# Kernel tuning notes

Hardware: AMD Instinct MI355X
Metric: run time of the kernel (lower is better)

The kernel has to match this reference:

```python
import jax, jax.numpy as jnp
import numpy as np

B, S, DIM = 1, 2048, 1024
HEADS, KV_HEADS, DH = 16, 2, 64
GQ = HEADS // KV_HEADS
CBS = 64   # compress block size
SBS = 64   # selection block size
NUM_SEL = 8
WIN = 512  # sliding window size
NUM_MEM = 1
SCALE = DH ** -0.5
NEG = -jnp.finfo(jnp.float32).max


def setup_inputs():
    ks = jax.random.split(jax.random.key(0), 12)
    cdim = CBS * DH
    dim_inner = HEADS * DH
    dim_kv = KV_HEADS * DH
    p = lambda k, shape: jax.random.normal(k, shape, jnp.float32) * 0.02
    return {
        "x": jax.random.normal(ks[0], (B, S, DIM), jnp.float32),
        "rms_g": jnp.ones((DIM,), jnp.float32),
        "W_qkv": p(ks[1], (DIM, dim_inner + 2 * dim_kv)),
        "k_pos": p(ks[2], (KV_HEADS, CBS, DH)),
        "v_pos": p(ks[3], (KV_HEADS, CBS, DH)),
        "mem_kv": p(ks[4], (2, KV_HEADS, NUM_MEM, DH)),
        "kW1": p(ks[5], (cdim, cdim)), "kb1": jnp.zeros((cdim,), jnp.float32),
        "kW2": p(ks[6], (cdim, DH)), "kb2": jnp.zeros((DH,), jnp.float32),
        "vW1": p(ks[7], (cdim, cdim)), "vb1": jnp.zeros((cdim,), jnp.float32),
        "vW2": p(ks[8], (cdim, DH)), "vb2": jnp.zeros((DH,), jnp.float32),
        "W_comb": p(ks[9], (DIM, 3 * HEADS)),
        "b_comb": jnp.tile(jnp.array([-2.0, -2.0, 2.0], jnp.float32), HEADS),
        "W_out": p(ks[10], (HEADS * DH, DIM)),
    }


def _rot_half(u):
    v = u.reshape(u.shape[:-1] + (DH // 2, 2))
    return jnp.stack([-v[..., 1], v[..., 0]], axis=-1).reshape(u.shape)


def reference(x, rms_g, W_qkv, k_pos, v_pos, mem_kv, kW1, kb1, kW2, kb2,
              vW1, vb1, vW2, vb2, W_comb, b_comb, W_out):
    n_cb = S // CBS
    n_fb = S // SBS
    num_sel = min(NUM_SEL, n_cb)

    # RMSNorm
    xn = x * jax.lax.rsqrt(jnp.mean(x * x, -1, keepdims=True) + jnp.finfo(jnp.float32).eps) * rms_g

    qkv = xn @ W_qkv
    q, k, v = jnp.split(qkv, [HEADS * DH, (HEADS + KV_HEADS) * DH], axis=-1)
    q = q.reshape(B, S, HEADS, DH).transpose(0, 2, 1, 3)       # b h n d
    k = k.reshape(B, S, KV_HEADS, DH).transpose(0, 2, 1, 3)
    v = v.reshape(B, S, KV_HEADS, DH).transpose(0, 2, 1, 3)

    # ---- compressed branch: per-block MLP compression of K/V ----
    kc = (k + jnp.tile(k_pos, (1, n_cb, 1))[None]).reshape(B, KV_HEADS, n_cb, CBS * DH)
    vc = (v + jnp.tile(v_pos, (1, n_cb, 1))[None]).reshape(B, KV_HEADS, n_cb, CBS * DH)
    ck = jax.nn.relu(kc @ kW1 + kb1) @ kW2 + kb2               # b h w d
    cv = jax.nn.relu(vc @ vW1 + vb1) @ vW2 + vb2
    ck = jnp.concatenate([jnp.broadcast_to(mem_kv[0], (B, KV_HEADS, NUM_MEM, DH)), ck], axis=2)
    cv = jnp.concatenate([jnp.broadcast_to(mem_kv[1], (B, KV_HEADS, NUM_MEM, DH)), cv], axis=2)
    ck_seq = jnp.concatenate([jnp.full((NUM_MEM,), -1), (jnp.arange(n_cb) + 1) * CBS - 1])
    cmask = ck_seq[None, :] < jnp.arange(S)[:, None]           # [S, mem+n_cb]
    qg = q.reshape(B, KV_HEADS, GQ, S, DH)
    csim = jnp.einsum('bhgid,bhjd->bhgij', qg, ck) * SCALE
    csim = jnp.where(cmask, csim, NEG)
    c_out = jnp.einsum('bhgij,bhjd->bhgid', jax.nn.softmax(csim, -1), cv).reshape(B, HEADS, S, DH)

    # ---- rotary embedding (interleaved pairs, theta=10000) ----
    inv_freq = 1.0 / (10000.0 ** (jnp.arange(0, DH, 2, dtype=jnp.float32) / DH))
    freqs = jnp.repeat(jnp.arange(S, dtype=jnp.float32)[:, None] * inv_freq, 2, axis=-1)
    cos, sin = jnp.cos(freqs), jnp.sin(freqs)
    rq = q * cos + _rot_half(q) * sin
    rk = k * cos + _rot_half(k) * sin

    # ---- block selection from compressed attention scores ----
    imp = csim[..., NUM_MEM:].mean(axis=2)                     # mean over grouped queries: [B,KVH,S,n_cb]
    imp = jnp.concatenate([jnp.full(imp.shape[:-1] + (1,), -1000.0), imp], -1)
    imp = jax.nn.softmax(imp, -1)[..., 1:]
    sel_val, sel_idx = jax.lax.top_k(imp, num_sel)             # [B,KVH,S,sel]
    fmask = jnp.broadcast_to((sel_val > 1e-10)[..., None], (B, KV_HEADS, S, num_sel, SBS))
    diag_idx = jnp.broadcast_to((jnp.arange(S) // SBS)[None, None, :, None], (B, KV_HEADS, S, 1))
    sel_idx = jnp.concatenate([sel_idx, diag_idx], -1)         # append own (diagonal) block
    causal = jnp.tril(jnp.ones((SBS, SBS), bool))
    diag_mask = jnp.broadcast_to(jnp.tile(causal, (n_fb, 1))[None, None, :, None, :], (B, KV_HEADS, S, 1, SBS))
    fmask = jnp.concatenate([fmask, diag_mask], axis=-2).reshape(B, KV_HEADS, S, (num_sel + 1) * SBS)

    # ---- fine attention over gathered selected blocks ----
    fkb = rk.reshape(B, KV_HEADS, 1, n_fb, SBS, DH)
    fvb = v.reshape(B, KV_HEADS, 1, n_fb, SBS, DH)
    gi = sel_idx[..., None, None]                              # [B,KVH,S,sel+1,1,1]
    fk = jnp.take_along_axis(fkb, gi, axis=3).reshape(B, KV_HEADS, S, (num_sel + 1) * SBS, DH)
    fv = jnp.take_along_axis(fvb, gi, axis=3).reshape(B, KV_HEADS, S, (num_sel + 1) * SBS, DH)
    fqg = rq.reshape(B, KV_HEADS, GQ, S, DH)
    fsim = jnp.einsum('bhgid,bhijd->bhgij', fqg, fk) * SCALE
    fsim = jnp.where(fmask[:, :, None], fsim, NEG)
    f_out = jnp.einsum('bhgij,bhijd->bhgid', jax.nn.softmax(fsim, -1), fv).reshape(B, HEADS, S, DH)

    # ---- causal sliding window (exact window, look_backward=1) ----
    skf = jnp.repeat(rk, GQ, axis=1)
    svf = jnp.repeat(v, GQ, axis=1)
    nw = S // WIN
    kw = skf.reshape(B, HEADS, nw, WIN, DH)
    vw = svf.reshape(B, HEADS, nw, WIN, DH)
    kcat = jnp.concatenate([jnp.pad(kw, ((0, 0), (0, 0), (1, 0), (0, 0), (0, 0)))[:, :, :nw], kw], axis=3)
    vcat = jnp.concatenate([jnp.pad(vw, ((0, 0), (0, 0), (1, 0), (0, 0), (0, 0)))[:, :, :nw], vw], axis=3)
    qw = rq.reshape(B, HEADS, nw, WIN, DH)
    gq_pos = jnp.arange(nw)[:, None, None] * WIN + jnp.arange(WIN)[None, :, None]
    gk_pos = jnp.arange(nw)[:, None, None] * WIN - WIN + jnp.arange(2 * WIN)[None, None, :]
    smask = (gk_pos >= 0) & (gk_pos <= gq_pos) & (gq_pos - gk_pos <= WIN)
    ssim = jnp.where(smask, jnp.einsum('bhwid,bhwjd->bhwij', qw, kcat) * SCALE, NEG)
    s_out = jnp.einsum('bhwij,bhwjd->bhwid', jax.nn.softmax(ssim, -1), vcat).reshape(B, HEADS, S, DH)

    # ---- learned per-token, per-head strategy combination ----
    gates = jax.nn.sigmoid(xn @ W_comb + b_comb).reshape(B, S, HEADS, 3).transpose(0, 2, 1, 3)
    out = gates[..., 0:1] * c_out + gates[..., 1:2] * f_out + gates[..., 2:3] * s_out
    return out.transpose(0, 2, 1, 3).reshape(B, S, HEADS * DH) @ W_out
```

## Files before the change

kernel.cpp:

```cpp
#include <hip/hip_runtime.h>
#include <hip/hip_bf16.h>
#include <cstddef>
#include <cstdint>

#define S      2048
#define DIM    1024
#define HEADS  16
#define KVH    2
#define GQ     8
#define DH     64
#define CBS    64
#define SBS    64
#define NUMSEL 8
#define WIN    512
#define NCB    (S / CBS)
#define CDIM   (CBS * DH)
#define QKVC   (HEADS * DH + 2 * KVH * DH)
#define KOFF   (HEADS * DH)
#define VOFF   (HEADS * DH + KVH * DH)
#define SCALE  0.125f
#define RMS_EPS 1.1920928955078125e-07f

typedef __attribute__((ext_vector_type(8))) short bf16x8;
typedef __attribute__((ext_vector_type(4))) float f32x4;
// ... 140 lines not shown
            if (gn >= N) continue;
            #pragma unroll
            for (int r = 0; r < 4; r++) {
                int gm = bm + m0 + i * 16 + quad * 4 + r;
                float v = acc[i][j][r];
                if (bias) v += bias[gn];
                if (ACT == 2) v = 1.f / (1.f + expf(-v));
                C[(size_t)gm * N + gn] = v;
            }
        }
    }
}

template <int BM, int BN, int WM, int WN>
__global__ __launch_bounds__(256) void gemm_mfma_kernel(
        const __hip_bfloat16* __restrict__ A, const float* __restrict__ B,
        float* __restrict__ C, int M, int N, int K, int kslice) {
    constexpr int BK = 32;
    constexpr int TM = BM / (WM * 16);
    constexpr int TN = BN / (WN * 16);
    constexpr int LDK = BK + 8;
    constexpr int NB = BN * BK / 256;
    __shared__ __hip_bfloat16 As[BM][LDK];
    __shared__ __hip_bfloat16 Bs[BN][LDK];
    int tid = threadIdx.x;
    int wave = tid >> 6, lane = tid & 63;
    int wm = wave % WM, wn = wave / WM;
    int m0 = wm * TM * 16, n0 = wn * TN * 16;
    int bm = blockIdx.y * BM, bn = blockIdx.x * BN;
    int kbeg = blockIdx.z * kslice, kend = kbeg + kslice;
    int lm = lane & 15, quad = lane >> 4;
    f32x4 acc[TM][TN] = {};
    for (int k0 = kbeg; k0 < kend; k0 += BK) {
        #pragma unroll
        for (int e = 0; e < BM * BK / (256 * 8); e++) {
            int idx = (tid + e * 256) * 8;
            int r = idx >> 5, kk = idx & 31;
            *(bf16x8*)(&As[r][kk]) =
                *(const bf16x8*)(A + (size_t)(bm + r) * K + k0 + kk);
        }
        float tmpB[NB];
        #pragma unroll
        for (int e = 0; e < NB; e++) {
            int idx = tid + e * 256;
            int kk = idx / BN, n = idx % BN;
            tmpB[e] = B[(size_t)(k0 + kk) * N + bn + n];
        }
        #pragma unroll
        for (int e = 0; e < NB; e++) {
            int idx = tid + e * 256;
            int kk = idx / BN, n = idx % BN;
            Bs[n][kk] = __float2bfloat16(tmpB[e]);
        }
        __syncthreads();
        bf16x8 af[TM], bf_[TN];
        #pragma unroll
        for (int i = 0; i < TM; i++)
            af[i] = *(const bf16x8*)(&As[m0 + i * 16 + lm][quad * 8]);
        #pragma unroll
        for (int j = 0; j < TN; j++)
            bf_[j] = *(const bf16x8*)(&Bs[n0 + j * 16 + lm][quad * 8]);
        #pragma unroll
        for (int i = 0; i < TM; i++)
            #pragma unroll
            for (int j = 0; j < TN; j++)
                acc[i][j] = __builtin_amdgcn_mfma_f32_16x16x32_bf16(
                    af[i], bf_[j], acc[i][j], 0, 0, 0);
        __syncthreads();
    }
    size_t cbase = (size_t)blockIdx.z * M * N;
    #pragma unroll
    for (int i = 0; i < TM; i++) {
        #pragma unroll
        for (int j = 0; j < TN; j++) {
            int gn = bn + n0 + j * 16 + lm;
            #pragma unroll
            for (int r = 0; r < 4; r++) {
                int gm = bm + m0 + i * 16 + quad * 4 + r;
                C[cbase + (size_t)gm * N + gn] = acc[i][j][r];
            }
        }
    }
}

__global__ __launch_bounds__(256) void gemm_splitk_kernel(
        const float* __restrict__ A, const float* __restrict__ B,
        float* __restrict__ P, int M, int N, int K, int kslice) {
    const int BM = 64, BN = 64, BK = 16;
    __shared__ float As[BK][BM + 4];
    __shared__ float Bs[BK][BN];
    int bm = blockIdx.y * BM, bn = blockIdx.x * BN;
    int z = blockIdx.z;
    int kbeg = z * kslice, kend = kbeg + kslice;
    int tid = threadIdx.x;
    int tx = tid & 15, ty = tid >> 4;
    float acc[4][4] = {{0.f}};
    for (int k0 = kbeg; k0 < kend; k0 += BK) {
        #pragma unroll
        for (int e = 0; e < 4; e++) {
            int idx = tid + e * 256;
            int m = idx >> 4, kk = idx & 15;
            int gm = bm + m;
            As[kk][m] = (gm < M) ? A[(size_t)gm * K + k0 + kk] : 0.f;
        }
        #pragma unroll
        for (int e = 0; e < 4; e++) {
            int idx = tid + e * 256;
            int kk = idx >> 6, n = idx & 63;
            int gn = bn + n;
            Bs[kk][n] = (gn < N) ? B[(size_t)(k0 + kk) * N + gn] : 0.f;
        }
        __syncthreads();
        #pragma unroll
        for (int kk = 0; kk < BK; kk++) {
            float a[4], b[4];
            #pragma unroll
            for (int i = 0; i < 4; i++) a[i] = As[kk][ty * 4 + i];
            #pragma unroll
            for (int j = 0; j < 4; j++) b[j] = Bs[kk][tx * 4 + j];
            #pragma unroll
            for (int i = 0; i < 4; i++)
                #pragma unroll
                for (int j = 0; j < 4; j++) acc[i][j] += a[i] * b[j];
        }
        __syncthreads();
    }
    #pragma unroll
    for (int i = 0; i < 4; i++) {
        int gm = bm + ty * 4 + i;
        if (gm >= M) continue;
        #pragma unroll
        for (int j = 0; j < 4; j++) {
            int gn = bn + tx * 4 + j;
            if (gn >= N) continue;
            P[((size_t)z * M + gm) * N + gn] = acc[i][j];
        }
    }
}

template <int ACT>
__global__ __launch_bounds__(256) void reduce_splitk_kernel(
        const float* __restrict__ P, const float* __restrict__ bias,
        float* __restrict__ C, int MN, int N, int splits) {
    int e = blockIdx.x * 256 + threadIdx.x;
    if (e >= MN) return;
    float s = 0.f;
    for (int z = 0; z < splits; z++) s += P[(size_t)z * MN + e];
    s += bias[e % N];
    if (ACT == 1) s = fmaxf(s, 0.f);
    C[e] = s;
}

__global__ __launch_bounds__(256) void rotary_kernel(
        const float* __restrict__ qkv, float* __restrict__ rq, float* __restrict__ rk,
        short* __restrict__ rkb) {
    int s = blockIdx.x, tid = threadIdx.x;
    for (int p = tid; p < (HEADS + KVH) * (DH / 2); p += 256) {
        int t; const float* src; float* dst; short* dst2 = nullptr;
        if (p < HEADS * (DH / 2)) {
            int h = p >> 5; t = p & 31;
            src = qkv + (size_t)s * QKVC + h * DH + 2 * t;
            dst = rq + (size_t)s * (HEADS * DH) + h * DH + 2 * t;
        } else {
            int pp = p - HEADS * (DH / 2);
            int h = pp >> 5; t = pp & 31;
            src = qkv + (size_t)s * QKVC + KOFF + h * DH + 2 * t;
            dst = rk + (size_t)s * (KVH * DH) + h * DH + 2 * t;
            dst2 = rkb + (size_t)s * (KVH * DH) + h * DH + 2 * t;
        }
        float u0 = src[0], u1 = src[1];
        float freq = powf(10000.f, -((float)(2 * t) / (float)DH));
        float ang = (float)s * freq;
        float sn, cs;
        sincosf(ang, &sn, &cs);
        float o0 = u0 * cs - u1 * sn;
        float o1 = u1 * cs + u0 * sn;
        dst[0] = o0;
        dst[1] = o1;
        if (dst2) { dst2[0] = f2bs(o0); dst2[1] = f2bs(o1); }
    }
}

__global__ __launch_bounds__(256) void build_cmat_kernel(
        const float* __restrict__ qkv, const float* __restrict__ k_pos,
        const float* __restrict__ v_pos, __hip_bfloat16* __restrict__ kcm,
        __hip_bfloat16* __restrict__ vcm) {
    int r = blockIdx.x;
    int h = r >> 5, w = r & 31;
    for (int e = threadIdx.x; e < CDIM; e += 256) {
        int i = e >> 6, d = e & 63;
        size_t qb = (size_t)(w * CBS + i) * QKVC;
        kcm[(size_t)r * CDIM + e] =
            __float2bfloat16(qkv[qb + KOFF + h * DH + d] + k_pos[(h * CBS + i) * DH + d]);
        vcm[(size_t)r * CDIM + e] =
            __float2bfloat16(qkv[qb + VOFF + h * DH + d] + v_pos[(h * CBS + i) * DH + d]);
    }
}

__global__ __launch_bounds__(256) void assemble_kernel(
        const float* __restrict__ ckb, const float* __restrict__ cvb,
        const float* __restrict__ mem_kv, float* __restrict__ ck, float* __restrict__ cv) {
    int e = blockIdx.x * 256 + threadIdx.x;
    if (e >= KVH * (NCB + 1) * DH) return;
    int d = e & 63;
    int j = (e >> 6) % (NCB + 1);
    int h = e / ((NCB + 1) * DH);
    if (j == 0) {
        ck[e] = mem_kv[0 * KVH * DH + h * DH + d];
        cv[e] = mem_kv[1 * KVH * DH + h * DH + d];
    } else {
        ck[e] = ckb[((size_t)h * NCB + j - 1) * DH + d];
        cv[e] = cvb[((size_t)h * NCB + j - 1) * DH + d];
    }
}

__global__ __launch_bounds__(64) void imp_kernel(
        const float* __restrict__ qkv, const float* __restrict__ ck,
        float* __restrict__ imp) {
    int kvh = blockIdx.x, s = blockIdx.y, t = threadIdx.x;
    __shared__ float qg[GQ * DH];
    __shared__ float ckl[NCB * 65];
    for (int e = t; e < GQ * DH; e += 64) {
        int g = e >> 6, d = e & 63;
        qg[e] = qkv[(size_t)s * QKVC + (kvh * GQ + g) * DH + d];
    }
    for (int e = t; e < NCB * DH; e += 64) {
        int w = e >> 6, d = e & 63;
        ckl[w * 65 + d] = ck[((size_t)kvh * (NCB + 1) + 1 + w) * DH + d];
    }
    __syncthreads();
    if (t < NCB) {
        int w = t;
        float val;
        if (w * CBS + CBS - 1 < s) {
            float acc = 0.f;
            #pragma unroll
            for (int g = 0; g < GQ; g++) {
                const float* qp = qg + g * DH;
                const float* cp = ckl + w * 65;
                #pragma unroll 16
                for (int d = 0; d < DH; d++) acc += qp[d] * cp[d];
            }
            val = acc * SCALE * (1.f / (float)GQ);
        } else {
            val = -INFINITY;
        }
        imp[((size_t)kvh * S + s) * NCB + w] = val;
    }
}

__global__ __launch_bounds__(256) void select_kernel(
        const float* __restrict__ imp, int* __restrict__ sel) {
    int idx = blockIdx.x * 256 + threadIdx.x;
    if (idx >= KVH * S) return;
    const float* row = imp + (size_t)idx * NCB;
    float p[NCB];
    float m = -1000.f;
    for (int w = 0; w < NCB; w++) { p[w] = row[w]; m = fmaxf(m, p[w]); }
    float z = expf(-1000.f - m);
    for (int w = 0; w < NCB; w++) { p[w] = expf(p[w] - m); z += p[w]; }
    float inv = 1.f / z;
    bool used[NCB];
    for (int w = 0; w < NCB; w++) used[w] = false;
    for (int i = 0; i < NUMSEL; i++) {
        int best = 0; float bv = -1.f;
        for (int w = 0; w < NCB; w++) {
            if (!used[w]) {
                float pw = p[w] * inv;
                if (pw > bv) { bv = pw; best = w; }
            }
        }
        used[best] = true;
        sel[(size_t)idx * NUMSEL + i] = (bv > 1e-10f) ? best : -1;
    }
}

__global__ __launch_bounds__(256) void cattn_kernel(
        const float* __restrict__ qkv, const float* __restrict__ ck,
        const float* __restrict__ cv, const float* __restrict__ gates,
        float* __restrict__ attn) {
    int h = blockIdx.x, qb = blockIdx.y;
    int kvh = h >> 3;
    int tid = threadIdx.x;
    int tx = tid & 15, ty = tid >> 4;
    __shared__ float Qs[64][68];
    __shared__ float Ks[64][68];
    __shared__ float Vs[64][68];
    auto& Ps = Ks;
    for (int e = tid; e < 4096; e += 256) {
        int q = e >> 6, d = e & 63;
        Qs[d][q] = qkv[(size_t)(qb * 64 + q) * QKVC + h * DH + d];
    }
    for (int e = tid; e < 4096; e += 256) {
        int j = e >> 6, d = e & 63;
        float kvl = 0.f, vvl = 0.f;
        if (j < NCB + 1) {
            kvl = ck[((size_t)kvh * (NCB + 1) + j) * DH + d];
            vvl = cv[((size_t)kvh * (NCB + 1) + j) * DH + d];
        }
        Ks[d][j] = kvl;
        Vs[j][d] = vvl;
    }
    __syncthreads();
    float sc[4][4] = {{0.f}};
    for (int d = 0; d < 64; d++) {
        float4 av = *(const float4*)&Qs[d][ty * 4];
        float4 bv = *(const float4*)&Ks[d][tx * 4];
        float a[4] = {av.x, av.y, av.z, av.w};
        float b[4] = {bv.x, bv.y, bv.z, bv.w};
        #pragma unroll
        for (int i = 0; i < 4; i++)
            #pragma unroll
            for (int j = 0; j < 4; j++) sc[i][j] += a[i] * b[j];
    }
    __syncthreads();
    float l[4];
    float pv4[4][4];
    #pragma unroll
    for (int i = 0; i < 4; i++) {
        int spos = qb * 64 + ty * 4 + i;
        float tm = -INFINITY;
        #pragma unroll
        for (int j = 0; j < 4; j++) {
            int jj = tx * 4 + j;
            bool vis = (jj == 0) || ((jj <= NCB) && (jj * 64 <= spos));
            sc[i][j] = vis ? sc[i][j] * SCALE : -INFINITY;
            tm = fmaxf(tm, sc[i][j]);
        }
        #pragma unroll
        for (int o = 1; o < 16; o <<= 1) tm = fmaxf(tm, __shfl_xor(tm, o));
        float rs = 0.f;
        #pragma unroll
        for (int j = 0; j < 4; j++) {
            float p = expf(sc[i][j] - tm);
            pv4[i][j] = p;
            rs += p;
        }
        #pragma unroll
        for (int o = 1; o < 16; o <<= 1) rs += __shfl_xor(rs, o);
        l[i] = rs;
    }
    #pragma unroll
    for (int j = 0; j < 4; j++) {
        float4 w = make_float4(pv4[0][j], pv4[1][j], pv4[2][j], pv4[3][j]);
        *(float4*)&Ps[tx * 4 + j][ty * 4] = w;
    }
    __syncthreads();
    float acc[4][4] = {{0.f}};
    for (int jj = 0; jj < 64; jj++) {
        float4 av = *(const float4*)&Ps[jj][ty * 4];
        float4 bv = *(const float4*)&Vs[jj][tx * 4];
        float a[4] = {av.x, av.y, av.z, av.w};
        float b[4] = {bv.x, bv.y, bv.z, bv.w};
        #pragma unroll
        for (int i = 0; i < 4; i++)
            #pragma unroll
            for (int j = 0; j < 4; j++) acc[i][j] += a[i] * b[j];
    }
    #pragma unroll
    for (int i = 0; i < 4; i++) {
        int spos = qb * 64 + ty * 4 + i;
        float g0 = gates[((size_t)spos * HEADS + h) * 3 + 0];
        float sca = g0 / l[i];
        #pragma unroll
        for (int j = 0; j < 4; j++)
            attn[(size_t)spos * (HEADS * DH) + h * DH + tx * 4 + j] = acc[i][j] * sca;
    }
}

__global__ __launch_bounds__(256) void fattn_kernel(
        const float* __restrict__ rq, const short* __restrict__ rkb,
        const short* __restrict__ vb, const int* __restrict__ sel,
        const float* __restrict__ gates, float* __restrict__ attn) {
    int kvh = blockIdx.x, s = blockIdx.y;
    int tid = threadIdx.x;
    int wv = tid >> 6, lane = tid & 63;
    int lm = lane & 15, quad = lane >> 4;
    int hh = tid >> 5, lk = tid & 31;
    __shared__ short Qb[16][68];
    __shared__ short Vt[64][68];
    __shared__ short Pb[16][68];
    __shared__ float Sc[8][68];
    __shared__ float alph[8], fac[8];
    __shared__ int bl[9];
    for (int e = tid; e < 512; e += 256) {
        int h = e >> 6, d = e & 63;
        Qb[h][d] = f2bs(rq[(size_t)s * (HEADS * DH) + (kvh * 8 + h) * DH + d]);
    }
    if (tid < NUMSEL) bl[tid] = sel[((size_t)kvh * S + s) * NUMSEL + tid];
    if (tid == NUMSEL) bl[NUMSEL] = s >> 6;
    __syncthreads();
    bf16x8 aq0 = *(const bf16x8*)&Qb[lm][quad * 8];
    bf16x8 aq1 = *(const bf16x8*)&Qb[lm][32 + quad * 8];
    float mh = -INFINITY, lh = 0.f;
    f32x4 oacc = {0.f, 0.f, 0.f, 0.f};
    for (int i = 0; i < 9; i++) {
        int w = bl[i];
        if (i < NUMSEL && w < 0) continue;
        #pragma unroll
        for (int r = 0; r < 2; r++) {
            int idx = tid + r * 256;
            int c8 = idx >> 6, j = idx & 63;
            bf16x8 vv = *(const bf16x8*)(vb + ((size_t)(w * SBS + j) * KVH + kvh) * DH + c8 * 8);
            #pragma unroll
            for (int t = 0; t < 8; t++) Vt[c8 * 8 + t][j] = vv[t];
        }
        {
            const short* kp = rkb + ((size_t)(w * SBS + wv * 16 + lm) * KVH + kvh) * DH;
            bf16x8 bk0 = *(const bf16x8*)(kp + quad * 8);
            bf16x8 bk1 = *(const bf16x8*)(kp + 32 + quad * 8);
            f32x4 sc4 = {0.f, 0.f, 0.f, 0.f};
            sc4 = __builtin_amdgcn_mfma_f32_16x16x32_bf16(aq0, bk0, sc4, 0, 0, 0);
            sc4 = __builtin_amdgcn_mfma_f32_16x16x32_bf16(aq1, bk1, sc4, 0, 0, 0);
            bool vis = (i < NUMSEL) || (wv * 16 + lm <= (s & 63));
            #pragma unroll
            for (int r = 0; r < 4; r++) {
                int row = quad * 4 + r;
                if (row < 8) Sc[row][wv * 16 + lm] = vis ? sc4[r] * SCALE : -INFINITY;
            }
        }
        __syncthreads();
        {
            float s0 = Sc[hh][lk], s1 = Sc[hh][lk + 32];
            float bmx = fmaxf(s0, s1);
            #pragma unroll
            for (int o = 1; o < 32; o <<= 1) bmx = fmaxf(bmx, __shfl_xor(bmx, o));
            float mn = fmaxf(mh, bmx);
            float scl = expf(mh - mn);
            float p0 = expf(s0 - mn), p1 = expf(s1 - mn);
            float rs = p0 + p1;
            #pragma unroll
            for (int o = 1; o < 32; o <<= 1) rs += __shfl_xor(rs, o);
            lh = lh * scl + rs;
            mh = mn;
            Pb[hh][lk] = f2bs(p0);
            Pb[hh][lk + 32] = f2bs(p1);
            if (lk == 0) alph[hh] = scl;
        }
        __syncthreads();
        {
            bf16x8 ap0 = *(const bf16x8*)&Pb[lm][quad * 8];
            bf16x8 ap1 = *(const bf16x8*)&Pb[lm][32 + quad * 8];
            bf16x8 bv0 = *(const bf16x8*)&Vt[wv * 16 + lm][quad * 8];
            bf16x8 bv1 = *(const bf16x8*)&Vt[wv * 16 + lm][32 + quad * 8];
            #pragma unroll
            for (int r = 0; r < 4; r++) oacc[r] *= alph[(quad * 4 + r) & 7];
            oacc = __builtin_amdgcn_mfma_f32_16x16x32_bf16(ap0, bv0, oacc, 0, 0, 0);
            oacc = __builtin_amdgcn_mfma_f32_16x16x32_bf16(ap1, bv1, oacc, 0, 0, 0);
        }
        __syncthreads();
    }
    if (lk == 0)
        fac[hh] = gates[((size_t)s * HEADS + kvh * 8 + hh) * 3 + 1] / lh;
    __syncthreads();
    #pragma unroll
    for (int r = 0; r < 4; r++) {
        int row = quad * 4 + r;
        if (row < 8)
            attn[(size_t)s * (HEADS * DH) + (kvh * 8 + row) * DH + wv * 16 + lm]
                += oacc[r] * fac[row];
    }
}

__global__ __launch_bounds__(256) void sattn_kernel(
        const float* __restrict__ rq, const float* __restrict__ rk,
        const float* __restrict__ qkv, const float* __restrict__ gates,
        float* __restrict__ attn) {
    int h = blockIdx.x, qb = blockIdx.y;
    int kvh = h >> 3;
    int tid = threadIdx.x;
    int tx = tid & 15, ty = tid >> 4;
    __shared__ float Qs[64][68];
    __shared__ float Ks[64][68];
    __shared__ float Vs[64][68];
    auto& Ps = Ks;
    for (int e = tid; e < 4096; e += 256) {
        int q = e >> 6, d = e & 63;
        Qs[d][q] = rq[(size_t)(qb * 64 + q) * (HEADS * DH) + h * DH + d];
    }
    float m[4], l[4], acc[4][4];
    #pragma unroll
    for (int i = 0; i < 4; i++) {
        m[i] = -INFINITY; l[i] = 0.f;
        #pragma unroll
        for (int j = 0; j < 4; j++) acc[i][j] = 0.f;
    }
    __syncthreads();
    for (int c = 0; c < 9; c++) {
        int kb = qb * 64 - WIN + c * 64;
        if (kb + 63 < 0) continue;
        for (int e = tid; e < 4096; e += 256) {
            int j = e >> 6, d = e & 63;
            int jpos = kb + j;
            float kvl = 0.f, vvl = 0.f;
            if (jpos >= 0) {
                kvl = rk[(size_t)jpos * (KVH * DH) + kvh * DH + d];
                vvl = qkv[(size_t)jpos * QKVC + VOFF + kvh * DH + d];
            }
            Ks[d][j] = kvl;
            Vs[j][d] = vvl;
        }
        __syncthreads();
        float sc[4][4] = {{0.f}};
        for (int d = 0; d < 64; d++) {
            float4 av = *(const float4*)&Qs[d][ty * 4];
            float4 bv = *(const float4*)&Ks[d][tx * 4];
            float a[4] = {av.x, av.y, av.z, av.w};
            float b[4] = {bv.x, bv.y, bv.z, bv.w};
            #pragma unroll
            for (int i = 0; i < 4; i++)
                #pragma unroll
                for (int j = 0; j < 4; j++) sc[i][j] += a[i] * b[j];
        }
        __syncthreads();
        float pv4[4][4];
        #pragma unroll
        for (int i = 0; i < 4; i++) {
            int spos = qb * 64 + ty * 4 + i;
            float tm = -INFINITY;
            #pragma unroll
            for (int j = 0; j < 4; j++) {
                int jpos = kb + tx * 4 + j;
                bool valid = (jpos >= 0) && (jpos <= spos) && (jpos >= spos - WIN);
                sc[i][j] = valid ? sc[i][j] * SCALE : -INFINITY;
                tm = fmaxf(tm, sc[i][j]);
            }
            #pragma unroll
            for (int o = 1; o < 16; o <<= 1) tm = fmaxf(tm, __shfl_xor(tm, o));
            float mn = fmaxf(m[i], tm);
            float sca = (mn == -INFINITY) ? 1.f : expf(m[i] - mn);
            float rs = 0.f;
            #pragma unroll
            for (int j = 0; j < 4; j++) {
                float p = (mn == -INFINITY) ? 0.f : expf(sc[i][j] - mn);
                pv4[i][j] = p;
                rs += p;
            }
            #pragma unroll
            for (int o = 1; o < 16; o <<= 1) rs += __shfl_xor(rs, o);
            l[i] = l[i] * sca + rs;
            m[i] = mn;
            #pragma unroll
            for (int j = 0; j < 4; j++) acc[i][j] *= sca;
        }
        #pragma unroll
        for (int j = 0; j < 4; j++) {
            float4 w = make_float4(pv4[0][j], pv4[1][j], pv4[2][j], pv4[3][j]);
            *(float4*)&Ps[tx * 4 + j][ty * 4] = w;
        }
        __syncthreads();
        for (int jj = 0; jj < 64; jj++) {
            float4 av = *(const float4*)&Ps[jj][ty * 4];
            float4 bv = *(const float4*)&Vs[jj][tx * 4];
            float a[4] = {av.x, av.y, av.z, av.w};
            float b[4] = {bv.x, bv.y, bv.z, bv.w};
            #pragma unroll
            for (int i = 0; i < 4; i++)
                #pragma unroll
                for (int j = 0; j < 4; j++) acc[i][j] += a[i] * b[j];
        }
        __syncthreads();
    }
    #pragma unroll
    for (int i = 0; i < 4; i++) {
        int spos = qb * 64 + ty * 4 + i;
        float g2 = gates[((size_t)spos * HEADS + h) * 3 + 2];
        float sca = g2 / l[i];
        #pragma unroll
        for (int j = 0; j < 4; j++)
            attn[(size_t)spos * (HEADS * DH) + h * DH + tx * 4 + j] += acc[i][j] * sca;
    }
}

extern "C" void kernel_launch(void* const* d_in, const int* in_sizes, int n_in,
                              void* d_out, int out_size, void* d_ws, size_t ws_size,
                              hipStream_t stream) {
    const float* x      = (const float*)d_in[0];
    const float* rms_g  = (const float*)d_in[1];
    const float* W_qkv  = (const float*)d_in[2];
    const float* k_pos  = (const float*)d_in[3];
    const float* v_pos  = (const float*)d_in[4];
    const float* mem_kv = (const float*)d_in[5];
    const float* kW1    = (const float*)d_in[6];
    const float* kb1    = (const float*)d_in[7];
    const float* kW2    = (const float*)d_in[8];
    const float* kb2    = (const float*)d_in[9];
    const float* vW1    = (const float*)d_in[10];
    const float* vb1    = (const float*)d_in[11];
    const float* vW2    = (const float*)d_in[12];
    const float* vb2    = (const float*)d_in[13];
    const float* W_comb = (const float*)d_in[14];
    const float* b_comb = (const float*)d_in[15];
    const float* W_out  = (const float*)d_in[16];
    float* out = (float*)d_out;

    float* ws    = (float*)d_ws;
    float* xn    = ws;
    float* qkv   = xn    + (size_t)S * DIM;
    float* rq    = qkv   + (size_t)S * QKVC;
    float* rk    = rq    + (size_t)S * HEADS * DH;
    float* R     = rk    + (size_t)S * KVH * DH;
    float* ck    = R     + 1048576;
    float* cv    = ck    + (size_t)KVH * (NCB + 1) * DH;
    float* imp   = cv    + (size_t)KVH * (NCB + 1) * DH;
    float* gates = imp   + (size_t)KVH * S * NCB;
    float* attn  = gates + (size_t)S * HEADS * 3;
    int*   sel   = (int*)(attn + (size_t)S * HEADS * DH);
    float* WT    = attn + (size_t)S * HEADS * DH + 32768;
    short* wqkvT = (short*)WT;
    short* woutT = (short*)(WT + 655360);
    short* wcombT= (short*)(WT + 655360 + 524288);

    __hip_bfloat16* xnb   = (__hip_bfloat16*)R;
    __hip_bfloat16* kcmb  = (__hip_bfloat16*)R;
    __hip_bfloat16* vcmb  = (__hip_bfloat16*)(R + 131072);
    float* khid  = R + 262144;
    float* vhid  = R + 524288;
    float* ckb   = R + 786432;
    float* cvb   = R + 790528;
    short* rkb   = (short*)(R + 794624);
    __hip_bfloat16* attnb = (__hip_bfloat16*)R;
    short* vbb   = (short*)imp;
    float* partW1 = attn;
    float* partW2 = imp;

    transpose_cast_kernel<<<dim3(QKVC / 64, DIM / 64), 256, 0, stream>>>(W_qkv, wqkvT, DIM, QKVC);
    transpose_cast_kernel<<<dim3(DIM / 64, DIM / 64), 256, 0, stream>>>(W_out, woutT, DIM, DIM);
    transpose_cast_kernel<<<dim3(1, DIM / 64), 256, 0, stream>>>(W_comb, wcombT, DIM, HEADS * 3);
    rmsnorm_kernel<<<S, 256, 0, stream>>>(x, rms_g, xn, xnb);
    gemm_bt_kernel<64, 64, 2, 2, 0><<<dim3(QKVC / 64, S / 64), 256, 0, stream>>>(
        xnb, wqkvT, nullptr, qkv, S, QKVC, DIM);
    gemm_bt_kernel<64, 64, 2, 2, 2><<<dim3(1, S / 64), 256, 0, stream>>>(
        xnb, wcombT, b_comb, gates, S, HEADS * 3, DIM);
    rotary_kernel<<<S, 256, 0, stream>>>(qkv, rq, rk, rkb);
    build_cmat_kernel<<<KVH * NCB, 256, 0, stream>>>(qkv, k_pos, v_pos, kcmb, vcmb);
    gemm_mfma_kernel<64, 128, 1, 4><<<dim3(CDIM / 128, 1, 8), 256, 0, stream>>>(
        kcmb, kW1, partW1, 64, CDIM, CDIM, CDIM / 8);
    reduce_splitk_kernel<1><<<(64 * CDIM + 255) / 256, 256, 0, stream>>>(
        partW1, kb1, khid, 64 * CDIM, CDIM, 8);
    gemm_splitk_kernel<<<dim3(1, 1, 32), 256, 0, stream>>>(khid, kW2, partW2, 64, DH, CDIM, CDIM / 32);
    reduce_splitk_kernel<0><<<(64 * DH + 255) / 256, 256, 0, stream>>>(partW2, kb2, ckb, 64 * DH, DH, 32);
    gemm_mfma_kernel<64, 128, 1, 4><<<dim3(CDIM / 128, 1, 8), 256, 0, stream>>>(
        vcmb, vW1, partW1, 64, CDIM, CDIM, CDIM / 8);
    reduce_splitk_kernel<1><<<(64 * CDIM + 255) / 256, 256, 0, stream>>>(
        partW1, vb1, vhid, 64 * CDIM, CDIM, 8);
    gemm_splitk_kernel<<<dim3(1, 1, 32), 256, 0, stream>>>(vhid, vW2, partW2, 64, DH, CDIM, CDIM / 32);
    reduce_splitk_kernel<0><<<(64 * DH + 255) / 256, 256, 0, stream>>>(partW2, vb2, cvb, 64 * DH, DH, 32);
    assemble_kernel<<<(KVH * (NCB + 1) * DH + 255) / 256, 256, 0, stream>>>(ckb, cvb, mem_kv, ck, cv);
    imp_kernel<<<dim3(KVH, S), 64, 0, stream>>>(qkv, ck, imp);
    select_kernel<<<(KVH * S + 255) / 256, 256, 0, stream>>>(imp, sel);
    cast_v_kernel<<<(S * KVH * DH / 4 + 255) / 256, 256, 0, stream>>>(qkv, vbb);
    cattn_kernel<<<dim3(HEADS, S / 64), 256, 0, stream>>>(qkv, ck, cv, gates, attn);
    fattn_kernel<<<dim3(KVH, S), 256, 0, stream>>>(rq, rkb, vbb, sel, gates, attn);
    sattn_kernel<<<dim3(HEADS, S / 64), 256, 0, stream>>>(rq, rk, qkv, gates, attn);
    cast_bf16_kernel<<<(S * HEADS * DH / 4 + 255) / 256, 256, 0, stream>>>(
        attn, attnb, S * HEADS * DH / 4);
    gemm_bt_kernel<64, 64, 2, 2, 0><<<dim3(DIM / 64, S / 64), 256, 0, stream>>>(
        attnb, woutT, nullptr, out, S, DIM, DIM);
}
```

Before: 619.6 us.

## Move compressed and sliding-window attention to bf16 MFMA with bf16 rotary outputs

```diff
diff --git a/kernel.cpp b/kernel.cpp
--- a/kernel.cpp
+++ b/kernel.cpp
@@ -316,32 +316,27 @@
 }
 
 __global__ __launch_bounds__(256) void rotary_kernel(
-        const float* __restrict__ qkv, float* __restrict__ rq, float* __restrict__ rk,
-        short* __restrict__ rkb) {
+        const float* __restrict__ qkv, short* __restrict__ rqb, short* __restrict__ rkb) {
     int s = blockIdx.x, tid = threadIdx.x;
     for (int p = tid; p < (HEADS + KVH) * (DH / 2); p += 256) {
-        int t; const float* src; float* dst; short* dst2 = nullptr;
+        int t; const float* src; short* dst;
         if (p < HEADS * (DH / 2)) {
             int h = p >> 5; t = p & 31;
             src = qkv + (size_t)s * QKVC + h * DH + 2 * t;
-            dst = rq + (size_t)s * (HEADS * DH) + h * DH + 2 * t;
+            dst = rqb + (size_t)s * (HEADS * DH) + h * DH + 2 * t;
         } else {
             int pp = p - HEADS * (DH / 2);
             int h = pp >> 5; t = pp & 31;
             src = qkv + (size_t)s * QKVC + KOFF + h * DH + 2 * t;
-            dst = rk + (size_t)s * (KVH * DH) + h * DH + 2 * t;
-            dst2 = rkb + (size_t)s * (KVH * DH) + h * DH + 2 * t;
+            dst = rkb + (size_t)s * (KVH * DH) + h * DH + 2 * t;
         }
         float u0 = src[0], u1 = src[1];
         float freq = powf(10000.f, -((float)(2 * t) / (float)DH));
         float ang = (float)s * freq;
         float sn, cs;
         sincosf(ang, &sn, &cs);
-        float o0 = u0 * cs - u1 * sn;
-        float o1 = u1 * cs + u0 * sn;
-        dst[0] = o0;
-        dst[1] = o1;
-        if (dst2) { dst2[0] = f2bs(o0); dst2[1] = f2bs(o1); }
+        dst[0] = f2bs(u0 * cs - u1 * sn);
+        dst[1] = f2bs(u1 * cs + u0 * sn);
     }
 }
 
@@ -363,19 +358,23 @@
 
 __global__ __launch_bounds__(256) void assemble_kernel(
         const float* __restrict__ ckb, const float* __restrict__ cvb,
-        const float* __restrict__ mem_kv, float* __restrict__ ck, float* __restrict__ cv) {
+        const float* __restrict__ mem_kv, float* __restrict__ ck, float* __restrict__ cv,
+        short* __restrict__ ck16, short* __restrict__ cv16) {
     int e = blockIdx.x * 256 + threadIdx.x;
     if (e >= KVH * (NCB + 1) * DH) return;
     int d = e & 63;
     int j = (e >> 6) % (NCB + 1);
     int h = e / ((NCB + 1) * DH);
+    float kv, vv;
     if (j == 0) {
-        ck[e] = mem_kv[0 * KVH * DH + h * DH + d];
-        cv[e] = mem_kv[1 * KVH * DH + h * DH + d];
+        kv = mem_kv[0 * KVH * DH + h * DH + d];
+        vv = mem_kv[1 * KVH * DH + h * DH + d];
     } else {
-        ck[e] = ckb[((size_t)h * NCB + j - 1) * DH + d];
-        cv[e] = cvb[((size_t)h * NCB + j - 1) * DH + d];
-    }
+        kv = ckb[((size_t)h * NCB + j - 1) * DH + d];
+        vv = cvb[((size_t)h * NCB + j - 1) * DH + d];
+    }
+    ck[e] = kv; cv[e] = vv;
+    ck16[e] = f2bs(kv); cv16[e] = f2bs(vv);
 }
 
 __global__ __launch_bounds__(64) void imp_kernel(
@@ -440,100 +439,108 @@
 }
 
 __global__ __launch_bounds__(256) void cattn_kernel(
-        const float* __restrict__ qkv, const float* __restrict__ ck,
-        const float* __restrict__ cv, const float* __restrict__ gates,
+        const float* __restrict__ qkv, const short* __restrict__ ck16,
+        const short* __restrict__ cv16, const float* __restrict__ gates,
         float* __restrict__ attn) {
     int h = blockIdx.x, qb = blockIdx.y;
     int kvh = h >> 3;
     int tid = threadIdx.x;
-    int tx = tid & 15, ty = tid >> 4;
-    __shared__ float Qs[64][68];
-    __shared__ float Ks[64][68];
-    __shared__ float Vs[64][68];
-    auto& Ps = Ks;
-    for (int e = tid; e < 4096; e += 256) {
-        int q = e >> 6, d = e & 63;
-        Qs[d][q] = qkv[(size_t)(qb * 64 + q) * QKVC + h * DH + d];
-    }
-    for (int e = tid; e < 4096; e += 256) {
-        int j = e >> 6, d = e & 63;
-        float kvl = 0.f, vvl = 0.f;
+    int wv = tid >> 6, lane = tid & 63;
+    int lm = lane & 15, quad = lane >> 4;
+    __shared__ short Qb[64][72];
+    __shared__ short Ks[64][72];
+    __shared__ short Vt[64][72];
+    __shared__ short Pb[64][72];
+    for (int e = tid; e < 1024; e += 256) {
+        int q = e >> 4, d4 = (e & 15) * 4;
+        float4 v = *(const float4*)(qkv + (size_t)(qb * 64 + q) * QKVC + h * DH + d4);
+        Qb[q][d4 + 0] = f2bs(v.x); Qb[q][d4 + 1] = f2bs(v.y);
+        Qb[q][d4 + 2] = f2bs(v.z); Qb[q][d4 + 3] = f2bs(v.w);
+    }
+    for (int e = tid; e < 512; e += 256) {
+        int c8 = e >> 6, j = e & 63;
+        bf16x8 kv = {}, vv = {};
         if (j < NCB + 1) {
-            kvl = ck[((size_t)kvh * (NCB + 1) + j) * DH + d];
-            vvl = cv[((size_t)kvh * (NCB + 1) + j) * DH + d];
-        }
-        Ks[d][j] = kvl;
-        Vs[j][d] = vvl;
+            kv = *(const bf16x8*)(ck16 + ((size_t)kvh * (NCB + 1) + j) * DH + c8 * 8);
+            vv = *(const bf16x8*)(cv16 + ((size_t)kvh * (NCB + 1) + j) * DH + c8 * 8);
+        }
+        #pragma unroll
+        for (int t = 0; t < 8; t++) {
+            Ks[j][c8 * 8 + t] = kv[t];
+            Vt[c8 * 8 + t][j] = vv[t];
+        }
     }
     __syncthreads();
-    float sc[4][4] = {{0.f}};
-    for (int d = 0; d < 64; d++) {
-        float4 av = *(const float4*)&Qs[d][ty * 4];
-        float4 bv = *(const float4*)&Ks[d][tx * 4];
-        float a[4] = {av.x, av.y, av.z, av.w};
-        float b[4] = {bv.x, bv.y, bv.z, bv.w};
-        #pragma unroll
-        for (int i = 0; i < 4; i++)
-            #pragma unroll
-            for (int j = 0; j < 4; j++) sc[i][j] += a[i] * b[j];
-    }
+    bf16x8 aq0 = *(const bf16x8*)&Qb[wv * 16 + lm][quad * 8];
+    bf16x8 aq1 = *(const bf16x8*)&Qb[wv * 16 + lm][32 + quad * 8];
+    int vismax = (qb < NCB) ? qb : NCB;
+    f32x4 sc[4];
+    #pragma unroll
+    for (int t = 0; t < 4; t++) {
+        bf16x8 bk0 = *(const bf16x8*)&Ks[t * 16 + lm][quad * 8];
+        bf16x8 bk1 = *(const bf16x8*)&Ks[t * 16 + lm][32 + quad * 8];
+        f32x4 s4 = {0.f, 0.f, 0.f, 0.f};
+        s4 = __builtin_amdgcn_mfma_f32_16x16x32_bf16(aq0, bk0, s4, 0, 0, 0);
+        s4 = __builtin_amdgcn_mfma_f32_16x16x32_bf16(aq1, bk1, s4, 0, 0, 0);
+        sc[t] = s4;
+    }
+    float l[4];
+    float pr[4][4];
+    #pragma unroll
+    for (int r = 0; r < 4; r++) {
+        float mx = -INFINITY;
+        #pragma unroll
+        for (int t = 0; t < 4; t++) {
+            int jj = t * 16 + lm;
+            bool vis = (jj == 0) || (jj <= vismax);
+            float v = vis ? sc[t][r] * SCALE : -INFINITY;
+            sc[t][r] = v;
+            mx = fmaxf(mx, v);
+        }
+        #pragma unroll
+        for (int o = 1; o < 16; o <<= 1) mx = fmaxf(mx, __shfl_xor(mx, o));
+        float sum = 0.f;
+        #pragma unroll
+        for (int t = 0; t < 4; t++) {
+            float p = expf(sc[t][r] - mx);
+            pr[r][t] = p;
+            sum += p;
+        }
+        #pragma unroll
+        for (int o = 1; o < 16; o <<= 1) sum += __shfl_xor(sum, o);
+        l[r] = sum;
+    }
+    #pragma unroll
+    for (int r = 0; r < 4; r++)
+        #pragma unroll
+        for (int t = 0; t < 4; t++)
+            Pb[wv * 16 + quad * 4 + r][t * 16 + lm] = f2bs(pr[r][t]);
     __syncthreads();
-    float l[4];
-    float pv4[4][4];
-    #pragma unroll
-    for (int i = 0; i < 4; i++) {
-        int spos = qb * 64 + ty * 4 + i;
-        float tm = -INFINITY;
-        #pragma unroll
-        for (int j = 0; j < 4; j++) {
-            int jj = tx * 4 + j;
-            bool vis = (jj == 0) || ((jj <= NCB) && (jj * 64 <= spos));
-            sc[i][j] = vis ? sc[i][j] * SCALE : -INFINITY;
-            tm = fmaxf(tm, sc[i][j]);
-        }
-        #pragma unroll
-        for (int o = 1; o < 16; o <<= 1) tm = fmaxf(tm, __shfl_xor(tm, o));
-        float rs = 0.f;
-        #pragma unroll
-        for (int j = 0; j < 4; j++) {
-            float p = expf(sc[i][j] - tm);
-            pv4[i][j] = p;
-            rs += p;
-        }
-        #pragma unroll
-        for (int o = 1; o < 16; o <<= 1) rs += __shfl_xor(rs, o);
-        l[i] = rs;
-    }
-    #pragma unroll
-    for (int j = 0; j < 4; j++) {
-        float4 w = make_float4(pv4[0][j], pv4[1][j], pv4[2][j], pv4[3][j]);
-        *(float4*)&Ps[tx * 4 + j][ty * 4] = w;
-    }
-    __syncthreads();
-    float acc[4][4] = {{0.f}};
-    for (int jj = 0; jj < 64; jj++) {
-        float4 av = *(const float4*)&Ps[jj][ty * 4];
-        float4 bv = *(const float4*)&Vs[jj][tx * 4];
-        float a[4] = {av.x, av.y, av.z, av.w};
-        float b[4] = {bv.x, bv.y, bv.z, bv.w};
-        #pragma unroll
-        for (int i = 0; i < 4; i++)
-            #pragma unroll
-            for (int j = 0; j < 4; j++) acc[i][j] += a[i] * b[j];
-    }
-    #pragma unroll
-    for (int i = 0; i < 4; i++) {
-        int spos = qb * 64 + ty * 4 + i;
+    bf16x8 ap0 = *(const bf16x8*)&Pb[wv * 16 + lm][quad * 8];
+    bf16x8 ap1 = *(const bf16x8*)&Pb[wv * 16 + lm][32 + quad * 8];
+    f32x4 oacc[4];
+    #pragma unroll
+    for (int t = 0; t < 4; t++) {
+        bf16x8 bv0 = *(const bf16x8*)&Vt[t * 16 + lm][quad * 8];
+        bf16x8 bv1 = *(const bf16x8*)&Vt[t * 16 + lm][32 + quad * 8];
+        f32x4 a = {0.f, 0.f, 0.f, 0.f};
+        a = __builtin_amdgcn_mfma_f32_16x16x32_bf16(ap0, bv0, a, 0, 0, 0);
+        a = __builtin_amdgcn_mfma_f32_16x16x32_bf16(ap1, bv1, a, 0, 0, 0);
+        oacc[t] = a;
+    }
+    #pragma unroll
+    for (int r = 0; r < 4; r++) {
+        int spos = qb * 64 + wv * 16 + quad * 4 + r;
         float g0 = gates[((size_t)spos * HEADS + h) * 3 + 0];
-        float sca = g0 / l[i];
-        #pragma unroll
-        for (int j = 0; j < 4; j++)
-            attn[(size_t)spos * (HEADS * DH) + h * DH + tx * 4 + j] = acc[i][j] * sca;
+        float f = g0 / l[r];
+        #pragma unroll
+        for (int t = 0; t < 4; t++)
+            attn[(size_t)spos * (HEADS * DH) + h * DH + t * 16 + lm] = oacc[t][r] * f;
     }
 }
 
 __global__ __launch_bounds__(256) void fattn_kernel(
-        const float* __restrict__ rq, const short* __restrict__ rkb,
+        const short* __restrict__ rqb, const short* __restrict__ rkb,
         const short* __restrict__ vb, const int* __restrict__ sel,
         const float* __restrict__ gates, float* __restrict__ attn) {
     int kvh = blockIdx.x, s = blockIdx.y;
@@ -549,7 +556,7 @@
     __shared__ int bl[9];
     for (int e = tid; e < 512; e += 256) {
         int h = e >> 6, d = e & 63;
-        Qb[h][d] = f2bs(rq[(size_t)s * (HEADS * DH) + (kvh * 8 + h) * DH + d]);
+        Qb[h][d] = rqb[(size_t)s * (HEADS * DH) + (kvh * 8 + h) * DH + d];
     }
     if (tid < NUMSEL) bl[tid] = sel[((size_t)kvh * S + s) * NUMSEL + tid];
     if (tid == NUMSEL) bl[NUMSEL] = s >> 6;
@@ -627,112 +634,105 @@
 }
 
 __global__ __launch_bounds__(256) void sattn_kernel(
-        const float* __restrict__ rq, const float* __restrict__ rk,
-        const float* __restrict__ qkv, const float* __restrict__ gates,
+        const short* __restrict__ rqb, const short* __restrict__ rkb,
+        const short* __restrict__ vb, const float* __restrict__ gates,
         float* __restrict__ attn) {
     int h = blockIdx.x, qb = blockIdx.y;
     int kvh = h >> 3;
     int tid = threadIdx.x;
-    int tx = tid & 15, ty = tid >> 4;
-    __shared__ float Qs[64][68];
-    __shared__ float Ks[64][68];
-    __shared__ float Vs[64][68];
-    auto& Ps = Ks;
-    for (int e = tid; e < 4096; e += 256) {
-        int q = e >> 6, d = e & 63;
-        Qs[d][q] = rq[(size_t)(qb * 64 + q) * (HEADS * DH) + h * DH + d];
-    }
-    float m[4], l[4], acc[4][4];
-    #pragma unroll
-    for (int i = 0; i < 4; i++) {
-        m[i] = -INFINITY; l[i] = 0.f;
-        #pragma unroll
-        for (int j = 0; j < 4; j++) acc[i][j] = 0.f;
-    }
-    __syncthreads();
+    int wv = tid >> 6, lane = tid & 63;
+    int lm = lane & 15, quad = lane >> 4;
+    __shared__ short Vt[64][72];
+    __shared__ short Pb[64][72];
+    const short* qp = rqb + (size_t)(qb * 64 + wv * 16 + lm) * (HEADS * DH) + h * DH;
+    bf16x8 aq0 = *(const bf16x8*)(qp + quad * 8);
+    bf16x8 aq1 = *(const bf16x8*)(qp + 32 + quad * 8);
+    int myrow = wv * 16 + quad * 4;
+    float m[4], l[4];
+    f32x4 oacc[4];
+    #pragma unroll
+    for (int r = 0; r < 4; r++) { m[r] = -INFINITY; l[r] = 0.f; }
+    #pragma unroll
+    for (int t = 0; t < 4; t++) oacc[t] = (f32x4){0.f, 0.f, 0.f, 0.f};
     for (int c = 0; c < 9; c++) {
         int kb = qb * 64 - WIN + c * 64;
-        if (kb + 63 < 0) continue;
-        for (int e = tid; e < 4096; e += 256) {
-            int j = e >> 6, d = e & 63;
-            int jpos = kb + j;
-            float kvl = 0.f, vvl = 0.f;
-            if (jpos >= 0) {
-                kvl = rk[(size_t)jpos * (KVH * DH) + kvh * DH + d];
-                vvl = qkv[(size_t)jpos * QKVC + VOFF + kvh * DH + d];
+        if (kb < 0) continue;
+        for (int e = tid; e < 512; e += 256) {
+            int c8 = e >> 6, j = e & 63;
+            bf16x8 vv = *(const bf16x8*)(vb + ((size_t)(kb + j) * KVH + kvh) * DH + c8 * 8);
+            #pragma unroll
+            for (int t = 0; t < 8; t++) Vt[c8 * 8 + t][j] = vv[t];
+        }
+        f32x4 sc[4];
+        #pragma unroll
+        for (int t = 0; t < 4; t++) {
+            const short* kp = rkb + ((size_t)(kb + t * 16 + lm) * KVH + kvh) * DH;
+            bf16x8 bk0 = *(const bf16x8*)(kp + quad * 8);
+            bf16x8 bk1 = *(const bf16x8*)(kp + 32 + quad * 8);
+            f32x4 s4 = {0.f, 0.f, 0.f, 0.f};
+            s4 = __builtin_amdgcn_mfma_f32_16x16x32_bf16(aq0, bk0, s4, 0, 0, 0);
+            s4 = __builtin_amdgcn_mfma_f32_16x16x32_bf16(aq1, bk1, s4, 0, 0, 0);
+            sc[t] = s4;
+        }
+        float pr[4][4];
+        #pragma unroll
+        for (int r = 0; r < 4; r++) {
+            int row = myrow + r;
+            float mx = -INFINITY;
+            #pragma unroll
+            for (int t = 0; t < 4; t++) {
+                int jj = t * 16 + lm;
+                bool vis = true;
+                if (c == 0) vis = (jj >= row);
+                if (c == 8) vis = (jj <= row);
+                float v = vis ? sc[t][r] * SCALE : -INFINITY;
+                sc[t][r] = v;
+                mx = fmaxf(mx, v);
             }
-            Ks[d][j] = kvl;
-            Vs[j][d] = vvl;
-        }
-        __syncthreads();
-        float sc[4][4] = {{0.f}};
-        for (int d = 0; d < 64; d++) {
-            float4 av = *(const float4*)&Qs[d][ty * 4];
-            float4 bv = *(const float4*)&Ks[d][tx * 4];
-            float a[4] = {av.x, av.y, av.z, av.w};
-            float b[4] = {bv.x, bv.y, bv.z, bv.w};
-            #pragma unroll
-            for (int i = 0; i < 4; i++)
-                #pragma unroll
-                for (int j = 0; j < 4; j++) sc[i][j] += a[i] * b[j];
-        }
-        __syncthreads();
-        float pv4[4][4];
-        #pragma unroll
-        for (int i = 0; i < 4; i++) {
-            int spos = qb * 64 + ty * 4 + i;
-            float tm = -INFINITY;
-            #pragma unroll
-            for (int j = 0; j < 4; j++) {
-                int jpos = kb + tx * 4 + j;
-                bool valid = (jpos >= 0) && (jpos <= spos) && (jpos >= spos - WIN);
-                sc[i][j] = valid ? sc[i][j] * SCALE : -INFINITY;
-                tm = fmaxf(tm, sc[i][j]);
+            #pragma unroll
+            for (int o = 1; o < 16; o <<= 1) mx = fmaxf(mx, __shfl_xor(mx, o));
+            float mn = fmaxf(m[r], mx);
+            float al = expf(m[r] - mn);
+            float sum = 0.f;
+            #pragma unroll
+            for (int t = 0; t < 4; t++) {
+                float p = expf(sc[t][r] - mn);
+                pr[r][t] = p;
+                sum += p;
             }
             #pragma unroll
-            for (int o = 1; o < 16; o <<= 1) tm = fmaxf(tm, __shfl_xor(tm, o));
-            float mn = fmaxf(m[i], tm);
-            float sca = (mn == -INFINITY) ? 1.f : expf(m[i] - mn);
-            float rs = 0.f;
-            #pragma unroll
-            for (int j = 0; j < 4; j++) {
-                float p = (mn == -INFINITY) ? 0.f : expf(sc[i][j] - mn);
-                pv4[i][j] = p;
-                rs += p;
-            }
-            #pragma unroll
-            for (int o = 1; o < 16; o <<= 1) rs += __shfl_xor(rs, o);
-            l[i] = l[i] * sca + rs;
-            m[i] = mn;
-            #pragma unroll
-            for (int j = 0; j < 4; j++) acc[i][j] *= sca;
-        }
-        #pragma unroll
-        for (int j = 0; j < 4; j++) {
-            float4 w = make_float4(pv4[0][j], pv4[1][j], pv4[2][j], pv4[3][j]);
-            *(float4*)&Ps[tx * 4 + j][ty * 4] = w;
-        }
-        __syncthreads();
-        for (int jj = 0; jj < 64; jj++) {
-            float4 av = *(const float4*)&Ps[jj][ty * 4];
-            float4 bv = *(const float4*)&Vs[jj][tx * 4];
-            float a[4] = {av.x, av.y, av.z, av.w};
-            float b[4] = {bv.x, bv.y, bv.z, bv.w};
-            #pragma unroll
-            for (int i = 0; i < 4; i++)
-                #pragma unroll
-                for (int j = 0; j < 4; j++) acc[i][j] += a[i] * b[j];
-        }
-        __syncthreads();
-    }
-    #pragma unroll
-    for (int i = 0; i < 4; i++) {
-        int spos = qb * 64 + ty * 4 + i;
+            for (int o = 1; o < 16; o <<= 1) sum += __shfl_xor(sum, o);
+            l[r] = l[r] * al + sum;
+            m[r] = mn;
+            #pragma unroll
+            for (int t = 0; t < 4; t++) oacc[t][r] *= al;
+        }
+        __syncthreads();
+        #pragma unroll
+        for (int r = 0; r < 4; r++)
+            #pragma unroll
+            for (int t = 0; t < 4; t++)
+                Pb[myrow + r][t * 16 + lm] = f2bs(pr[r][t]);
+        __syncthreads();
+        bf16x8 ap0 = *(const bf16x8*)&Pb[wv * 16 + lm][quad * 8];
+        bf16x8 ap1 = *(const bf16x8*)&Pb[wv * 16 + lm][32 + quad * 8];
+        #pragma unroll
+        for (int t = 0; t < 4; t++) {
+            bf16x8 bv0 = *(const bf16x8*)&Vt[t * 16 + lm][quad * 8];
+            bf16x8 bv1 = *(const bf16x8*)&Vt[t * 16 + lm][32 + quad * 8];
+            oacc[t] = __builtin_amdgcn_mfma_f32_16x16x32_bf16(ap0, bv0, oacc[t], 0, 0, 0);
+            oacc[t] = __builtin_amdgcn_mfma_f32_16x16x32_bf16(ap1, bv1, oacc[t], 0, 0, 0);
+        }
+        __syncthreads();
+    }
+    #pragma unroll
+    for (int r = 0; r < 4; r++) {
+        int spos = qb * 64 + myrow + r;
         float g2 = gates[((size_t)spos * HEADS + h) * 3 + 2];
-        float sca = g2 / l[i];
-        #pragma unroll
-        for (int j = 0; j < 4; j++)
-            attn[(size_t)spos * (HEADS * DH) + h * DH + tx * 4 + j] += acc[i][j] * sca;
+        float f = g2 / l[r];
+        #pragma unroll
+        for (int t = 0; t < 4; t++)
+            attn[(size_t)spos * (HEADS * DH) + h * DH + t * 16 + lm] += oacc[t][r] * f;
     }
 }
 
@@ -761,16 +761,18 @@
     float* ws    = (float*)d_ws;
     float* xn    = ws;
     float* qkv   = xn    + (size_t)S * DIM;
-    float* rq    = qkv   + (size_t)S * QKVC;
-    float* rk    = rq    + (size_t)S * HEADS * DH;
-    float* R     = rk    + (size_t)S * KVH * DH;
+    short* rqb   = (short*)(qkv + (size_t)S * QKVC);
+    short* rkb   = (short*)((float*)rqb + 1048576);
+    float* R     = (float*)rkb + 131072;
     float* ck    = R     + 1048576;
     float* cv    = ck    + (size_t)KVH * (NCB + 1) * DH;
-    float* imp   = cv    + (size_t)KVH * (NCB + 1) * DH;
+    short* ck16  = (short*)(cv + (size_t)KVH * (NCB + 1) * DH);
+    short* cv16  = (short*)((float*)ck16 + 2112);
+    float* imp   = (float*)cv16 + 2112;
     float* gates = imp   + (size_t)KVH * S * NCB;
     float* attn  = gates + (size_t)S * HEADS * 3;
     int*   sel   = (int*)(attn + (size_t)S * HEADS * DH);
-    float* WT    = attn + (size_t)S * HEADS * DH + 32768;
+    float* WT    = attn + (size_t)S * HEADS * DH + 8192;
     short* wqkvT = (short*)WT;
     short* woutT = (short*)(WT + 655360);
     short* wcombT= (short*)(WT + 655360 + 524288);
@@ -782,7 +784,6 @@
     float* vhid  = R + 524288;
     float* ckb   = R + 786432;
     float* cvb   = R + 790528;
-    short* rkb   = (short*)(R + 794624);
     __hip_bfloat16* attnb = (__hip_bfloat16*)R;
     short* vbb   = (short*)imp;
     float* partW1 = attn;
@@ -796,7 +797,7 @@
         xnb, wqkvT, nullptr, qkv, S, QKVC, DIM);
     gemm_bt_kernel<64, 64, 2, 2, 2><<<dim3(1, S / 64), 256, 0, stream>>>(
         xnb, wcombT, b_comb, gates, S, HEADS * 3, DIM);
-    rotary_kernel<<<S, 256, 0, stream>>>(qkv, rq, rk, rkb);
+    rotary_kernel<<<S, 256, 0, stream>>>(qkv, rqb, rkb);
     build_cmat_kernel<<<KVH * NCB, 256, 0, stream>>>(qkv, k_pos, v_pos, kcmb, vcmb);
     gemm_mfma_kernel<64, 128, 1, 4><<<dim3(CDIM / 128, 1, 8), 256, 0, stream>>>(
         kcmb, kW1, partW1, 64, CDIM, CDIM, CDIM / 8);
@@ -810,13 +811,14 @@
         partW1, vb1, vhid, 64 * CDIM, CDIM, 8);
     gemm_splitk_kernel<<<dim3(1, 1, 32), 256, 0, stream>>>(vhid, vW2, partW2, 64, DH, CDIM, CDIM / 32);
     reduce_splitk_kernel<0><<<(64 * DH + 255) / 256, 256, 0, stream>>>(partW2, vb2, cvb, 64 * DH, DH, 32);
-    assemble_kernel<<<(KVH * (NCB + 1) * DH + 255) / 256, 256, 0, stream>>>(ckb, cvb, mem_kv, ck, cv);
+    assemble_kernel<<<(KVH * (NCB + 1) * DH + 255) / 256, 256, 0, stream>>>(
+        ckb, cvb, mem_kv, ck, cv, ck16, cv16);
     imp_kernel<<<dim3(KVH, S), 64, 0, stream>>>(qkv, ck, imp);
     select_kernel<<<(KVH * S + 255) / 256, 256, 0, stream>>>(imp, sel);
     cast_v_kernel<<<(S * KVH * DH / 4 + 255) / 256, 256, 0, stream>>>(qkv, vbb);
-    cattn_kernel<<<dim3(HEADS, S / 64), 256, 0, stream>>>(qkv, ck, cv, gates, attn);
-    fattn_kernel<<<dim3(KVH, S), 256, 0, stream>>>(rq, rkb, vbb, sel, gates, attn);
-    sattn_kernel<<<dim3(HEADS, S / 64), 256, 0, stream>>>(rq, rk, qkv, gates, attn);
+    cattn_kernel<<<dim3(HEADS, S / 64), 256, 0, stream>>>(qkv, ck16, cv16, gates, attn);
+    fattn_kernel<<<dim3(KVH, S), 256, 0, stream>>>(rqb, rkb, vbb, sel, gates, attn);
+    sattn_kernel<<<dim3(HEADS, S / 64), 256, 0, stream>>>(rqb, rkb, vbb, gates, attn);
     cast_bf16_kernel<<<(S * HEADS * DH / 4 + 255) / 256, 256, 0, stream>>>(
         attn, attnb, S * HEADS * DH / 4);
     gemm_bt_kernel<64, 64, 2, 2, 0><<<dim3(DIM / 64, S / 64), 256, 0, stream>>>(
```

New measurement: 551.5 us. 1.12x faster.
